# Performance work log

Hardware: AMD Instinct MI355X
Metric: run time of the kernel (lower is better)

The kernel has to match this reference:

```python
import jax, jax.numpy as jnp
import numpy as np
from jax import lax

N_KERNELS = 10000
KS = 9
DILATIONS = (1, 2, 4, 8, 16)   # static dilation groups, 2000 kernels each
GROUP = N_KERNELS // len(DILATIONS)
BN_EPS = 1e-5


def setup_inputs() -> dict:
    key = jax.random.key(0)
    kx, kw, kb, klw = jax.random.split(key, 4)
    B, L, C, n_class = 16, 256, 3, 10
    x_enc = jax.random.normal(kx, (B, L, C), dtype=jnp.float32)
    # ROCKET kernels: normal weights, mean-centered per kernel
    W = jax.random.normal(kw, (N_KERNELS, C, KS), dtype=jnp.float32)
    W = W - W.mean(axis=(1, 2), keepdims=True)
    # ROCKET biases: uniform(-1, 1)
    b = jax.random.uniform(kb, (N_KERNELS,), dtype=jnp.float32) * 2.0 - 1.0
    gamma = jnp.ones((2 * N_KERNELS,), dtype=jnp.float32)
    beta = jnp.zeros((2 * N_KERNELS,), dtype=jnp.float32)
    linW = jax.random.normal(klw, (2 * N_KERNELS, n_class), dtype=jnp.float32) * 0.01
    linB = jnp.zeros((n_class,), dtype=jnp.float32)
    return {"x_enc": x_enc, "W": W, "b": b, "gamma": gamma, "beta": beta,
            "linW": linW, "linB": linB}


def _rocket_features(x, W, b):
    # x: [B, C, L]; W: [N_KERNELS, C, KS]; b: [N_KERNELS]
    feats = []
    dn = ("NCH", "OIH", "NCH")
    for i, d in enumerate(DILATIONS):
        w = W[i * GROUP:(i + 1) * GROUP]                       # [G, C, KS]
        bb = b[i * GROUP:(i + 1) * GROUP]                      # [G]
        y = lax.conv_general_dilated(x, w, window_strides=(1,),
                                     padding="SAME", rhs_dilation=(d,),
                                     dimension_numbers=dn)      # [B, G, L]
        y = y + bb[None, :, None]
        feats.append(y.max(axis=-1))                            # max pooling
        feats.append(jnp.where(y > 0, 1.0, 0.0).mean(axis=-1))  # PPV
    return jnp.concatenate(feats, axis=-1)                      # [B, 2*N_KERNELS]


def reference(x_enc, W, b, gamma, beta, linW, linB):
    x = jnp.transpose(x_enc, (0, 2, 1))        # [B, C, L]
    feat = _rocket_features(x, W, b)           # [B, 20000]
    # BatchNorm1d (training mode: batch statistics, biased variance)
    mu = feat.mean(axis=0)
    var = feat.var(axis=0)
    feat_n = (feat - mu) * lax.rsqrt(var + BN_EPS) * gamma + beta
    return feat_n @ linW + linB                # [B, num_class]
```

## Files before the change

### kernel.cpp

```cpp
#include <hip/hip_runtime.h>
#include <cmath>

#define NK       10000
#define GROUP    2000
#define SEQ_L    256
#define FEAT_DIM 20000
#define NBATCH   16

typedef _Float16 half8 __attribute__((ext_vector_type(8)));
typedef float    f32x4 __attribute__((ext_vector_type(4)));

__launch_bounds__(256)
__global__ void rocket_gemm(const float* __restrict__ x_enc,
                            const float* __restrict__ Wk,
                            const float* __restrict__ bias,
                            float* __restrict__ feat)
{
    __shared__ __align__(16) float    xp[3 * 384];
    __shared__ __align__(16) _Float16 Bh[1024 * 8];
    __shared__ __align__(16) _Float16 Bl[1024 * 8];

    const int mt  = blockIdx.x;
    const int gi  = blockIdx.y;
    const int b   = blockIdx.z;
    const int d   = 1 << gi;
    const int tid = threadIdx.x;
    const int l   = tid & 63;
    const int wv  = tid >> 6;
    const int kb  = l >> 4;
    const int lr  = l & 15;

    for (int i = tid; i < 3 * 384; i += 256) xp[i] = 0.f;
    __syncthreads();
    for (int e = tid; e < SEQ_L * 3; e += 256) {
        const int t = e / 3;
        const int c = e - t * 3;
        xp[c * 384 + 64 + t] = x_enc[(b * SEQ_L + t) * 3 + c];
    }

    half8 ahi[4], alo[4];
#pragma unroll
    for (int tt = 0; tt < 4; ++tt) {
        const int nl = mt * 256 + wv * 64 + tt * 16 + lr;
        const int n  = gi * GROUP + (nl < GROUP ? nl : GROUP - 1);
#pragma unroll
        for (int j = 0; j < 8; ++j) {
            const int k = kb * 8 + j;
            float w;
            if (k < 27)       w = Wk[n * 27 + k];
            else if (k == 27) w = bias[n];
            else              w = 0.f;
            const _Float16 h = (_Float16)w;
            ahi[tt][j] = h;
            alo[tt][j] = (_Float16)(w - (float)h);
        }
    }

    __syncthreads();

#pragma unroll
    for (int q = 0; q < 4; ++q) {
        const int idx = q * 256 + tid;
        const int kbb = idx >> 8;
        const int t   = idx & 255;
        half8 hv, lv;
#pragma unroll
        for (int kk = 0; kk < 8; ++kk) {
            const int k2 = kbb * 8 + kk;
            float v = 0.f;
            if (k2 < 27) {
                const int c  = (k2 >= 18) ? 2 : (k2 >= 9 ? 1 : 0);
                const int k9 = k2 - c * 9;
                v = xp[c * 384 + 64 + t + (k9 - 4) * d];
            } else if (k2 == 27) {
                v = 1.0f;
            }
            const _Float16 h = (_Float16)v;
            hv[kk] = h;
            lv[kk] = (_Float16)(v - (float)h);
        }
        *(half8*)&Bh[idx * 8] = hv;
        *(half8*)&Bl[idx * 8] = lv;
    }
    __syncthreads();

    float mx[4][4];
    int   cnt[4][4];
#pragma unroll
    for (int tt = 0; tt < 4; ++tt)
#pragma unroll
        for (int r = 0; r < 4; ++r) { mx[tt][r] = -INFINITY; cnt[tt][r] = 0; }

#pragma unroll
    for (int ch = 0; ch < 16; ++ch) {
        const int t = ch * 16 + lr;
        const half8 bh = *(const half8*)&Bh[(kb * 256 + t) * 8];
        const half8 bl = *(const half8*)&Bl[(kb * 256 + t) * 8];
#pragma unroll
        for (int tt = 0; tt < 4; ++tt) {
            f32x4 acc = {0.f, 0.f, 0.f, 0.f};
            acc = __builtin_amdgcn_mfma_f32_16x16x32_f16(ahi[tt], bh, acc, 0, 0, 0);
            acc = __builtin_amdgcn_mfma_f32_16x16x32_f16(alo[tt], bh, acc, 0, 0, 0);
            acc = __builtin_amdgcn_mfma_f32_16x16x32_f16(ahi[tt], bl, acc, 0, 0, 0);
#pragma unroll
            for (int r = 0; r < 4; ++r) {
                const float y = acc[r];
                mx[tt][r]   = fmaxf(mx[tt][r], y);
                cnt[tt][r] += (y > 0.f) ? 1 : 0;
            }
        }
    }

#pragma unroll
    for (int tt = 0; tt < 4; ++tt)
#pragma unroll
        for (int r = 0; r < 4; ++r) {
#pragma unroll
            for (int m = 1; m < 16; m <<= 1) {
                mx[tt][r]   = fmaxf(mx[tt][r], __shfl_xor(mx[tt][r], m));
                cnt[tt][r] += __shfl_xor(cnt[tt][r], m);
            }
        }

    if (lr == 0) {
        float* fb = feat + b * FEAT_DIM + gi * 4000;
#pragma unroll
        for (int tt = 0; tt < 4; ++tt)
#pragma unroll
            for (int r = 0; r < 4; ++r) {
                const int nl = mt * 256 + wv * 64 + tt * 16 + kb * 4 + r;
                if (nl < GROUP) {
                    fb[nl]        = mx[tt][r];
                    fb[2000 + nl] = (float)cnt[tt][r] * (1.0f / 256.0f);
                }
            }
    }
}

__launch_bounds__(256)
__global__ void bn_gemv(const float* __restrict__ feat,
                        const float* __restrict__ gamma,
                        const float* __restrict__ beta,
                        const float* __restrict__ linW,
                        float* __restrict__ partial)
{
    __shared__ float gs[125], hs[125];
    __shared__ float lw[125 * 10];
    const int sl  = blockIdx.x;
    const int f0  = sl * 125;
    const int tid = threadIdx.x;

    for (int i = tid; i < 1250; i += 256) lw[i] = linW[f0 * 10 + i];

    if (tid < 125) {
        const int f = f0 + tid;
        float s = 0.f, ss = 0.f;
#pragma unroll
        for (int b = 0; b < NBATCH; ++b) {
            const float v = feat[b * FEAT_DIM + f];
            s += v; ss += v * v;
        }
        const float mu  = s * (1.f / NBATCH);
        const float var = ss * (1.f / NBATCH) - mu * mu;
        const float gg  = gamma[f] * rsqrtf(var + 1e-5f);
        gs[tid] = gg;
        hs[tid] = beta[f] - mu * gg;
    }
    __syncthreads();

    const int bb = tid >> 4;
    const int ft = tid & 15;
    float acc[10];
#pragma unroll
    for (int c = 0; c < 10; ++c) acc[c] = 0.f;

    for (int i = ft; i < 125; i += 16) {
        const float tv = fmaf(feat[bb * FEAT_DIM + f0 + i], gs[i], hs[i]);
#pragma unroll
        for (int c = 0; c < 10; ++c) acc[c] = fmaf(tv, lw[i * 10 + c], acc[c]);
    }
#pragma unroll
    for (int c = 0; c < 10; ++c)
#pragma unroll
        for (int m = 1; m < 16; m <<= 1) acc[c] += __shfl_xor(acc[c], m);

    if (ft == 0) {
#pragma unroll
        for (int c = 0; c < 10; ++c)
            partial[(sl * NBATCH + bb) * 10 + c] = acc[c];
    }
}

__launch_bounds__(640)
__global__ void gemv_final(const float* __restrict__ partial,
                           const float* __restrict__ linB,
                           float* __restrict__ out)
{
    __shared__ float red[4][160];
    const int tid = threadIdx.x;
    const int q   = tid / 160;
    const int o   = tid - q * 160;
    float s = 0.f;
    for (int sl = q; sl < 160; sl += 4) s += partial[sl * 160 + o];
    red[q][o] = s;
    __syncthreads();
    if (tid < 160)
        out[tid] = red[0][tid] + red[1][tid] + red[2][tid] + red[3][tid]
                 + linB[tid % 10];
}

extern "C" void kernel_launch(void* const* d_in, const int* in_sizes, int n_in,
                              void* d_out, int out_size, void* d_ws, size_t ws_size,
                              hipStream_t stream) {
    const float* x     = (const float*)d_in[0];
    const float* Wk    = (const float*)d_in[1];
    const float* bias  = (const float*)d_in[2];
    const float* gamma = (const float*)d_in[3];
    const float* beta  = (const float*)d_in[4];
    const float* linW  = (const float*)d_in[5];
    const float* linB  = (const float*)d_in[6];
    float* out = (float*)d_out;

    float* feat    = (float*)d_ws;
    float* partial = feat + NBATCH * FEAT_DIM;

    rocket_gemm<<<dim3(8, 5, NBATCH), 256, 0, stream>>>(x, Wk, bias, feat);
    bn_gemv<<<dim3(160), 256, 0, stream>>>(feat, gamma, beta, linW, partial);
    gemv_final<<<dim3(1), 640, 0, stream>>>(partial, linB, out);
}
```

Measured before the change: 38.67 us.

## Fuse ROCKET convolution with BatchNorm and GEMV, looping batch per block

Merges the feature-extraction kernel and the BN+GEMV kernel into one. Each block owns 64 kernels of one dilation group and loops over all 16 batch samples, so batch statistics can be computed in shared memory and the feature matrix never goes to global memory. This removes one launch and the feature write and read-back. The cost is far fewer blocks (160 instead of 640) with a serial batch loop and extra barriers per sample, and input values are now read straight from global memory instead of a padded shared copy.

```diff
diff --git a/kernel.cpp b/kernel.cpp
--- a/kernel.cpp
+++ b/kernel.cpp
@@ -4,44 +4,41 @@
 #define NK       10000
 #define GROUP    2000
 #define SEQ_L    256
-#define FEAT_DIM 20000
 #define NBATCH   16
+#define MROWS    64
+#define NPBLK    160
 
 typedef _Float16 half8 __attribute__((ext_vector_type(8)));
 typedef float    f32x4 __attribute__((ext_vector_type(4)));
 
-__launch_bounds__(256)
-__global__ void rocket_gemm(const float* __restrict__ x_enc,
-                            const float* __restrict__ Wk,
-                            const float* __restrict__ bias,
-                            float* __restrict__ feat)
+__launch_bounds__(512)
+__global__ void rocket_fused(const float* __restrict__ x_enc,
+                             const float* __restrict__ Wk,
+                             const float* __restrict__ bias,
+                             const float* __restrict__ gamma,
+                             const float* __restrict__ beta,
+                             const float* __restrict__ linW,
+                             float* __restrict__ partial)
 {
-    __shared__ __align__(16) float    xp[3 * 384];
     __shared__ __align__(16) _Float16 Bh[1024 * 8];
     __shared__ __align__(16) _Float16 Bl[1024 * 8];
-
-    const int mt  = blockIdx.x;
-    const int gi  = blockIdx.y;
-    const int b   = blockIdx.z;
-    const int d   = 1 << gi;
-    const int tid = threadIdx.x;
-    const int l   = tid & 63;
-    const int wv  = tid >> 6;
-    const int kb  = l >> 4;
-    const int lr  = l & 15;
-
-    for (int i = tid; i < 3 * 384; i += 256) xp[i] = 0.f;
-    __syncthreads();
-    for (int e = tid; e < SEQ_L * 3; e += 256) {
-        const int t = e / 3;
-        const int c = e - t * 3;
-        xp[c * 384 + 64 + t] = x_enc[(b * SEQ_L + t) * 3 + c];
-    }
+    __shared__ float2 red[8][64];
+    __shared__ float2 fsm[64][16];
+    __shared__ float2 gh[128];
+
+    const int blk_m = blockIdx.x;
+    const int gi    = blockIdx.y;
+    const int d     = 1 << gi;
+    const int tid   = threadIdx.x;
+    const int l     = tid & 63;
+    const int wv    = tid >> 6;
+    const int kb    = l >> 4;
+    const int lr    = l & 15;
 
     half8 ahi[4], alo[4];
 #pragma unroll
     for (int tt = 0; tt < 4; ++tt) {
-        const int nl = mt * 256 + wv * 64 + tt * 16 + lr;
+        const int nl = blk_m * MROWS + tt * 16 + lr;
         const int n  = gi * GROUP + (nl < GROUP ? nl : GROUP - 1);
 #pragma unroll
         for (int j = 0; j < 8; ++j) {
@@ -56,138 +53,150 @@
         }
     }
 
-    __syncthreads();
-
-#pragma unroll
-    for (int q = 0; q < 4; ++q) {
-        const int idx = q * 256 + tid;
-        const int kbb = idx >> 8;
-        const int t   = idx & 255;
-        half8 hv, lv;
-#pragma unroll
-        for (int kk = 0; kk < 8; ++kk) {
-            const int k2 = kbb * 8 + kk;
-            float v = 0.f;
-            if (k2 < 27) {
-                const int c  = (k2 >= 18) ? 2 : (k2 >= 9 ? 1 : 0);
-                const int k9 = k2 - c * 9;
-                v = xp[c * 384 + 64 + t + (k9 - 4) * d];
-            } else if (k2 == 27) {
-                v = 1.0f;
-            }
-            const _Float16 h = (_Float16)v;
-            hv[kk] = h;
-            lv[kk] = (_Float16)(v - (float)h);
-        }
-        *(half8*)&Bh[idx * 8] = hv;
-        *(half8*)&Bl[idx * 8] = lv;
-    }
-    __syncthreads();
-
-    float mx[4][4];
-    int   cnt[4][4];
-#pragma unroll
-    for (int tt = 0; tt < 4; ++tt)
-#pragma unroll
-        for (int r = 0; r < 4; ++r) { mx[tt][r] = -INFINITY; cnt[tt][r] = 0; }
-
-#pragma unroll
-    for (int ch = 0; ch < 16; ++ch) {
-        const int t = ch * 16 + lr;
-        const half8 bh = *(const half8*)&Bh[(kb * 256 + t) * 8];
-        const half8 bl = *(const half8*)&Bl[(kb * 256 + t) * 8];
-#pragma unroll
-        for (int tt = 0; tt < 4; ++tt) {
-            f32x4 acc = {0.f, 0.f, 0.f, 0.f};
-            acc = __builtin_amdgcn_mfma_f32_16x16x32_f16(ahi[tt], bh, acc, 0, 0, 0);
-            acc = __builtin_amdgcn_mfma_f32_16x16x32_f16(alo[tt], bh, acc, 0, 0, 0);
-            acc = __builtin_amdgcn_mfma_f32_16x16x32_f16(ahi[tt], bl, acc, 0, 0, 0);
+    for (int b = 0; b < NBATCH; ++b) {
+        {
+            const int t  = tid & 255;
+            const int qh = tid >> 8;
+#pragma unroll
+            for (int qq = 0; qq < 2; ++qq) {
+                const int q = qh * 2 + qq;
+                half8 hv, lv;
+#pragma unroll
+                for (int kk = 0; kk < 8; ++kk) {
+                    const int k2 = q * 8 + kk;
+                    float v = 0.f;
+                    if (k2 < 27) {
+                        const int c  = k2 / 9;
+                        const int k9 = k2 - c * 9;
+                        const int t2 = t + (k9 - 4) * d;
+                        if (t2 >= 0 && t2 < SEQ_L)
+                            v = x_enc[(b * SEQ_L + t2) * 3 + c];
+                    } else if (k2 == 27) {
+                        v = 1.0f;
+                    }
+                    const _Float16 h = (_Float16)v;
+                    hv[kk] = h;
+                    lv[kk] = (_Float16)(v - (float)h);
+                }
+                *(half8*)&Bh[(q * 256 + t) * 8] = hv;
+                *(half8*)&Bl[(q * 256 + t) * 8] = lv;
+            }
+        }
+        __syncthreads();
+
+        float mx[4][4];
+        int   cnt[4][4];
+#pragma unroll
+        for (int tt = 0; tt < 4; ++tt)
+#pragma unroll
+            for (int r = 0; r < 4; ++r) { mx[tt][r] = -INFINITY; cnt[tt][r] = 0; }
+
+#pragma unroll
+        for (int ch = 0; ch < 2; ++ch) {
+            const int t = wv * 32 + ch * 16 + lr;
+            const half8 bh = *(const half8*)&Bh[(kb * 256 + t) * 8];
+            const half8 bl = *(const half8*)&Bl[(kb * 256 + t) * 8];
+#pragma unroll
+            for (int tt = 0; tt < 4; ++tt) {
+                f32x4 acc = {0.f, 0.f, 0.f, 0.f};
+                acc = __builtin_amdgcn_mfma_f32_16x16x32_f16(ahi[tt], bh, acc, 0, 0, 0);
+                acc = __builtin_amdgcn_mfma_f32_16x16x32_f16(alo[tt], bh, acc, 0, 0, 0);
+                acc = __builtin_amdgcn_mfma_f32_16x16x32_f16(ahi[tt], bl, acc, 0, 0, 0);
+#pragma unroll
+                for (int r = 0; r < 4; ++r) {
+                    const float y = acc[r];
+                    mx[tt][r]   = fmaxf(mx[tt][r], y);
+                    cnt[tt][r] += (y > 0.f) ? 1 : 0;
+                }
+            }
+        }
+
+#pragma unroll
+        for (int tt = 0; tt < 4; ++tt)
 #pragma unroll
             for (int r = 0; r < 4; ++r) {
-                const float y = acc[r];
-                mx[tt][r]   = fmaxf(mx[tt][r], y);
-                cnt[tt][r] += (y > 0.f) ? 1 : 0;
-            }
-        }
-    }
-
-#pragma unroll
-    for (int tt = 0; tt < 4; ++tt)
-#pragma unroll
-        for (int r = 0; r < 4; ++r) {
-#pragma unroll
-            for (int m = 1; m < 16; m <<= 1) {
-                mx[tt][r]   = fmaxf(mx[tt][r], __shfl_xor(mx[tt][r], m));
-                cnt[tt][r] += __shfl_xor(cnt[tt][r], m);
-            }
-        }
-
-    if (lr == 0) {
-        float* fb = feat + b * FEAT_DIM + gi * 4000;
-#pragma unroll
-        for (int tt = 0; tt < 4; ++tt)
-#pragma unroll
-            for (int r = 0; r < 4; ++r) {
-                const int nl = mt * 256 + wv * 64 + tt * 16 + kb * 4 + r;
-                if (nl < GROUP) {
-                    fb[nl]        = mx[tt][r];
-                    fb[2000 + nl] = (float)cnt[tt][r] * (1.0f / 256.0f);
+#pragma unroll
+                for (int m = 1; m < 16; m <<= 1) {
+                    mx[tt][r]   = fmaxf(mx[tt][r], __shfl_xor(mx[tt][r], m));
+                    cnt[tt][r] += __shfl_xor(cnt[tt][r], m);
                 }
             }
-    }
-}
-
-__launch_bounds__(256)
-__global__ void bn_gemv(const float* __restrict__ feat,
-                        const float* __restrict__ gamma,
-                        const float* __restrict__ beta,
-                        const float* __restrict__ linW,
-                        float* __restrict__ partial)
-{
-    __shared__ float gs[125], hs[125];
-    __shared__ float lw[125 * 10];
-    const int sl  = blockIdx.x;
-    const int f0  = sl * 125;
-    const int tid = threadIdx.x;
-
-    for (int i = tid; i < 1250; i += 256) lw[i] = linW[f0 * 10 + i];
-
-    if (tid < 125) {
-        const int f = f0 + tid;
+        if (lr == 0) {
+#pragma unroll
+            for (int tt = 0; tt < 4; ++tt)
+#pragma unroll
+                for (int r = 0; r < 4; ++r)
+                    red[wv][tt * 16 + kb * 4 + r] =
+                        make_float2(mx[tt][r], (float)cnt[tt][r]);
+        }
+        __syncthreads();
+
+        if (tid < MROWS) {
+            float fm = -INFINITY, fc = 0.f;
+#pragma unroll
+            for (int w = 0; w < 8; ++w) {
+                fm  = fmaxf(fm, red[w][tid].x);
+                fc += red[w][tid].y;
+            }
+            fsm[tid][b] = make_float2(fm, fc * (1.0f / 256.0f));
+        }
+        __syncthreads();
+    }
+
+    if (tid < 128) {
+        const int  rloc  = tid & 63;
+        const bool isppv = tid >= 64;
         float s = 0.f, ss = 0.f;
 #pragma unroll
         for (int b = 0; b < NBATCH; ++b) {
-            const float v = feat[b * FEAT_DIM + f];
+            const float v = isppv ? fsm[rloc][b].y : fsm[rloc][b].x;
             s += v; ss += v * v;
         }
         const float mu  = s * (1.f / NBATCH);
         const float var = ss * (1.f / NBATCH) - mu * mu;
-        const float gg  = gamma[f] * rsqrtf(var + 1e-5f);
-        gs[tid] = gg;
-        hs[tid] = beta[f] - mu * gg;
+        const int   nl  = blk_m * MROWS + rloc;
+        float gg = 0.f, hh = 0.f;
+        if (nl < GROUP) {
+            const int fg = gi * 4000 + (isppv ? 2000 : 0) + nl;
+            gg = gamma[fg] * rsqrtf(var + 1e-5f);
+            hh = beta[fg] - mu * gg;
+        }
+        gh[tid] = make_float2(gg, hh);
     }
     __syncthreads();
 
-    const int bb = tid >> 4;
-    const int ft = tid & 15;
-    float acc[10];
-#pragma unroll
-    for (int c = 0; c < 10; ++c) acc[c] = 0.f;
-
-    for (int i = ft; i < 125; i += 16) {
-        const float tv = fmaf(feat[bb * FEAT_DIM + f0 + i], gs[i], hs[i]);
-#pragma unroll
-        for (int c = 0; c < 10; ++c) acc[c] = fmaf(tv, lw[i * 10 + c], acc[c]);
-    }
-#pragma unroll
-    for (int c = 0; c < 10; ++c)
-#pragma unroll
-        for (int m = 1; m < 16; m <<= 1) acc[c] += __shfl_xor(acc[c], m);
-
-    if (ft == 0) {
+    {
+        const int bb = tid >> 5;
+        const int ft = tid & 31;
+        float acc[10];
+#pragma unroll
+        for (int c = 0; c < 10; ++c) acc[c] = 0.f;
+
+#pragma unroll
+        for (int fi = 0; fi < 4; ++fi) {
+            const int  f     = fi * 32 + ft;
+            const int  rloc  = f & 63;
+            const bool isppv = f >= 64;
+            const float  v  = isppv ? fsm[rloc][bb].y : fsm[rloc][bb].x;
+            const float2 G  = gh[f];
+            const float  tv = fmaf(v, G.x, G.y);
+            const int nl = blk_m * MROWS + rloc;
+            const int fg = gi * 4000 + (isppv ? 2000 : 0)
+                         + (nl < GROUP ? nl : GROUP - 1);
+#pragma unroll
+            for (int c = 0; c < 10; ++c)
+                acc[c] = fmaf(tv, linW[fg * 10 + c], acc[c]);
+        }
 #pragma unroll
         for (int c = 0; c < 10; ++c)
-            partial[(sl * NBATCH + bb) * 10 + c] = acc[c];
+#pragma unroll
+            for (int m = 1; m < 32; m <<= 1) acc[c] += __shfl_xor(acc[c], m);
+
+        if (ft == 0) {
+#pragma unroll
+            for (int c = 0; c < 10; ++c)
+                partial[((gi * 32 + blk_m) * NBATCH + bb) * 10 + c] = acc[c];
+        }
     }
 }
 
@@ -196,16 +205,16 @@
                            const float* __restrict__ linB,
                            float* __restrict__ out)
 {
-    __shared__ float red[4][160];
+    __shared__ float red2[4][160];
     const int tid = threadIdx.x;
     const int q   = tid / 160;
     const int o   = tid - q * 160;
     float s = 0.f;
-    for (int sl = q; sl < 160; sl += 4) s += partial[sl * 160 + o];
-    red[q][o] = s;
+    for (int sl = q; sl < NPBLK; sl += 4) s += partial[sl * 160 + o];
+    red2[q][o] = s;
     __syncthreads();
     if (tid < 160)
-        out[tid] = red[0][tid] + red[1][tid] + red[2][tid] + red[3][tid]
+        out[tid] = red2[0][tid] + red2[1][tid] + red2[2][tid] + red2[3][tid]
                  + linB[tid % 10];
 }
 
@@ -221,10 +230,9 @@
     const float* linB  = (const float*)d_in[6];
     float* out = (float*)d_out;
 
-    float* feat    = (float*)d_ws;
-    float* partial = feat + NBATCH * FEAT_DIM;
-
-    rocket_gemm<<<dim3(8, 5, NBATCH), 256, 0, stream>>>(x, Wk, bias, feat);
-    bn_gemv<<<dim3(160), 256, 0, stream>>>(feat, gamma, beta, linW, partial);
+    float* partial = (float*)d_ws;
+
+    rocket_fused<<<dim3(32, 5), 512, 0, stream>>>(x, Wk, bias, gamma, beta,
+                                                  linW, partial);
     gemv_final<<<dim3(1), 640, 0, stream>>>(partial, linB, out);
 }
```

After: 100.9 us. 161% more time.

## Split im2col B-matrix build into separate kernel and shrink GEMM blocks

Applied to the files above, without the earlier changes.

The fp16 hi/lo im2col operand is now built once per (dilation, batch) in its own kernel and written to global workspace, instead of every M-tile block rebuilding it in LDS. The GEMM kernel reads B directly from global/L2, uses 128-thread blocks with twice as many tiles, and splits the three MFMAs across two accumulators to shorten the dependency chain. This removes redundant B construction and LDS syncs, at the cost of an extra kernel launch and global-memory traffic for B.

```diff
diff --git a/kernel.cpp b/kernel.cpp
--- a/kernel.cpp
+++ b/kernel.cpp
@@ -11,37 +11,72 @@
 typedef float    f32x4 __attribute__((ext_vector_type(4)));
 
 __launch_bounds__(256)
-__global__ void rocket_gemm(const float* __restrict__ x_enc,
-                            const float* __restrict__ Wk,
-                            const float* __restrict__ bias,
-                            float* __restrict__ feat)
-{
-    __shared__ __align__(16) float    xp[3 * 384];
-    __shared__ __align__(16) _Float16 Bh[1024 * 8];
-    __shared__ __align__(16) _Float16 Bl[1024 * 8];
-
+__global__ void build_B(const float* __restrict__ x_enc,
+                        _Float16* __restrict__ Bh_g,
+                        _Float16* __restrict__ Bl_g)
+{
+    __shared__ __align__(16) float xp[3 * 384];
+    const int gi  = blockIdx.x;
+    const int b   = blockIdx.y;
+    const int d   = 1 << gi;
+    const int tid = threadIdx.x;
+
+    for (int i = tid; i < 3 * 384; i += 256) xp[i] = 0.f;
+    __syncthreads();
+    for (int e = tid; e < SEQ_L * 3; e += 256) {
+        const int t = e / 3;
+        const int c = e - t * 3;
+        xp[c * 384 + 64 + t] = x_enc[(b * SEQ_L + t) * 3 + c];
+    }
+    __syncthreads();
+
+    const int base = (gi * NBATCH + b) * 1024;
+#pragma unroll
+    for (int q = 0; q < 4; ++q) {
+        const int idx = q * 256 + tid;
+        const int kb  = idx >> 8;
+        const int t   = idx & 255;
+        half8 hv, lv;
+#pragma unroll
+        for (int kk = 0; kk < 8; ++kk) {
+            const int k2 = kb * 8 + kk;
+            float v = 0.f;
+            if (k2 < 27) {
+                const int c  = (k2 >= 18) ? 2 : (k2 >= 9 ? 1 : 0);
+                const int k9 = k2 - c * 9;
+                v = xp[c * 384 + 64 + t + (k9 - 4) * d];
+            } else if (k2 == 27) {
+                v = 1.0f;
+            }
+            const _Float16 h = (_Float16)v;
+            hv[kk] = h;
+            lv[kk] = (_Float16)(v - (float)h);
+        }
+        *(half8*)&Bh_g[(base + idx) * 8] = hv;
+        *(half8*)&Bl_g[(base + idx) * 8] = lv;
+    }
+}
+
+__launch_bounds__(128)
+__global__ void gemm_feat(const _Float16* __restrict__ Bh_g,
+                          const _Float16* __restrict__ Bl_g,
+                          const float* __restrict__ Wk,
+                          const float* __restrict__ bias,
+                          float* __restrict__ feat)
+{
     const int mt  = blockIdx.x;
     const int gi  = blockIdx.y;
     const int b   = blockIdx.z;
-    const int d   = 1 << gi;
     const int tid = threadIdx.x;
     const int l   = tid & 63;
     const int wv  = tid >> 6;
     const int kb  = l >> 4;
     const int lr  = l & 15;
 
-    for (int i = tid; i < 3 * 384; i += 256) xp[i] = 0.f;
-    __syncthreads();
-    for (int e = tid; e < SEQ_L * 3; e += 256) {
-        const int t = e / 3;
-        const int c = e - t * 3;
-        xp[c * 384 + 64 + t] = x_enc[(b * SEQ_L + t) * 3 + c];
-    }
-
     half8 ahi[4], alo[4];
 #pragma unroll
     for (int tt = 0; tt < 4; ++tt) {
-        const int nl = mt * 256 + wv * 64 + tt * 16 + lr;
+        const int nl = mt * 128 + wv * 64 + tt * 16 + lr;
         const int n  = gi * GROUP + (nl < GROUP ? nl : GROUP - 1);
 #pragma unroll
         for (int j = 0; j < 8; ++j) {
@@ -56,33 +91,8 @@
         }
     }
 
-    __syncthreads();
-
-#pragma unroll
-    for (int q = 0; q < 4; ++q) {
-        const int idx = q * 256 + tid;
-        const int kbb = idx >> 8;
-        const int t   = idx & 255;
-        half8 hv, lv;
-#pragma unroll
-        for (int kk = 0; kk < 8; ++kk) {
-            const int k2 = kbb * 8 + kk;
-            float v = 0.f;
-            if (k2 < 27) {
-                const int c  = (k2 >= 18) ? 2 : (k2 >= 9 ? 1 : 0);
-                const int k9 = k2 - c * 9;
-                v = xp[c * 384 + 64 + t + (k9 - 4) * d];
-            } else if (k2 == 27) {
-                v = 1.0f;
-            }
-            const _Float16 h = (_Float16)v;
-            hv[kk] = h;
-            lv[kk] = (_Float16)(v - (float)h);
-        }
-        *(half8*)&Bh[idx * 8] = hv;
-        *(half8*)&Bl[idx * 8] = lv;
-    }
-    __syncthreads();
+    const _Float16* bhp = Bh_g + ((gi * NBATCH + b) * 1024 + kb * 256) * 8;
+    const _Float16* blp = Bl_g + ((gi * NBATCH + b) * 1024 + kb * 256) * 8;
 
     float mx[4][4];
     int   cnt[4][4];
@@ -94,17 +104,18 @@
 #pragma unroll
     for (int ch = 0; ch < 16; ++ch) {
         const int t = ch * 16 + lr;
-        const half8 bh = *(const half8*)&Bh[(kb * 256 + t) * 8];
-        const half8 bl = *(const half8*)&Bl[(kb * 256 + t) * 8];
+        const half8 bh = *(const half8*)&bhp[t * 8];
+        const half8 bl = *(const half8*)&blp[t * 8];
 #pragma unroll
         for (int tt = 0; tt < 4; ++tt) {
-            f32x4 acc = {0.f, 0.f, 0.f, 0.f};
-            acc = __builtin_amdgcn_mfma_f32_16x16x32_f16(ahi[tt], bh, acc, 0, 0, 0);
-            acc = __builtin_amdgcn_mfma_f32_16x16x32_f16(alo[tt], bh, acc, 0, 0, 0);
-            acc = __builtin_amdgcn_mfma_f32_16x16x32_f16(ahi[tt], bl, acc, 0, 0, 0);
+            f32x4 acc1 = {0.f, 0.f, 0.f, 0.f};
+            f32x4 acc2 = {0.f, 0.f, 0.f, 0.f};
+            acc1 = __builtin_amdgcn_mfma_f32_16x16x32_f16(ahi[tt], bh, acc1, 0, 0, 0);
+            acc2 = __builtin_amdgcn_mfma_f32_16x16x32_f16(ahi[tt], bl, acc2, 0, 0, 0);
+            acc1 = __builtin_amdgcn_mfma_f32_16x16x32_f16(alo[tt], bh, acc1, 0, 0, 0);
 #pragma unroll
             for (int r = 0; r < 4; ++r) {
-                const float y = acc[r];
+                const float y = acc1[r] + acc2[r];
                 mx[tt][r]   = fmaxf(mx[tt][r], y);
                 cnt[tt][r] += (y > 0.f) ? 1 : 0;
             }
@@ -128,7 +139,7 @@
         for (int tt = 0; tt < 4; ++tt)
 #pragma unroll
             for (int r = 0; r < 4; ++r) {
-                const int nl = mt * 256 + wv * 64 + tt * 16 + kb * 4 + r;
+                const int nl = mt * 128 + wv * 64 + tt * 16 + kb * 4 + r;
                 if (nl < GROUP) {
                     fb[nl]        = mx[tt][r];
                     fb[2000 + nl] = (float)cnt[tt][r] * (1.0f / 256.0f);
@@ -221,10 +232,13 @@
     const float* linB  = (const float*)d_in[6];
     float* out = (float*)d_out;
 
-    float* feat    = (float*)d_ws;
-    float* partial = feat + NBATCH * FEAT_DIM;
-
-    rocket_gemm<<<dim3(8, 5, NBATCH), 256, 0, stream>>>(x, Wk, bias, feat);
+    float*    feat    = (float*)d_ws;
+    float*    partial = feat + NBATCH * FEAT_DIM;
+    _Float16* Bh      = (_Float16*)(partial + 160 * 160);
+    _Float16* Bl      = Bh + 5 * NBATCH * 1024 * 8;
+
+    build_B<<<dim3(5, NBATCH), 256, 0, stream>>>(x, Bh, Bl);
+    gemm_feat<<<dim3(16, 5, NBATCH), 128, 0, stream>>>(Bh, Bl, Wk, bias, feat);
     bn_gemv<<<dim3(160), 256, 0, stream>>>(feat, gamma, beta, linW, partial);
     gemv_final<<<dim3(1), 640, 0, stream>>>(partial, linB, out);
 }
```

After: 44.89 us. 1.16x slower.
